# Kernel tuning notes

Hardware: AMD Instinct MI355X
Metric: run time of the kernel (lower is better)

## Reference

```python
import jax, jax.numpy as jnp
import numpy as np

L, B, Q, P, D, H, F = 3, 256, 128, 16, 256, 16, 512
DK = D // H
SCALE = DK ** -0.5  # lsa=False -> constant scale
EPS = 1e-5


def _ln(x, g, b):
    m = jnp.mean(x, axis=-1, keepdims=True)
    v = jnp.mean(jnp.square(x - m), axis=-1, keepdims=True)
    return (x - m) * jax.lax.rsqrt(v + EPS) * g + b


def setup_inputs() -> dict:
    key = jax.random.key(0)
    ks = jax.random.split(key, 12)
    w = lambda k, shape: 0.02 * jax.random.normal(k, shape, dtype=jnp.float32)
    return {
        "x": jax.random.normal(ks[0], (B, Q, P), dtype=jnp.float32),
        "attn_bias": 0.1 * jax.random.normal(ks[1], (1, Q, Q), dtype=jnp.float32),
        "W_P": w(ks[2], (P, D)), "b_P": jnp.zeros((D,), jnp.float32),
        "W_pos": w(ks[3], (Q, D)),
        "Wq": w(ks[4], (L, D, D)), "bq": jnp.zeros((L, D), jnp.float32),
        "Wk": w(ks[5], (L, D, D)), "bk": jnp.zeros((L, D), jnp.float32),
        "Wv": w(ks[6], (L, D, D)), "bv": jnp.zeros((L, D), jnp.float32),
        "Wo": w(ks[7], (L, D, D)), "bo": jnp.zeros((L, D), jnp.float32),
        "ln1_g": jnp.ones((L, D), jnp.float32), "ln1_b": jnp.zeros((L, D), jnp.float32),
        "W1": w(ks[8], (L, D, F)), "b1": jnp.zeros((L, F), jnp.float32),
        "W2": w(ks[9], (L, F, D)), "b2": jnp.zeros((L, D), jnp.float32),
        "ln2_g": jnp.ones((L, D), jnp.float32), "ln2_b": jnp.zeros((L, D), jnp.float32),
    }


def _encoder(x, attn_bias, W_P, b_P, W_pos,
             Wq, bq, Wk, bk, Wv, bv, Wo, bo, ln1_g, ln1_b,
             W1, b1, W2, b2, ln2_g, ln2_b):
    # patch embedding + positional encoding (dropout=0, eval mode)
    z = x @ W_P + b_P + W_pos                      # [B, Q, D]
    bias = attn_bias[:, None]                      # [1, 1, Q, Q]

    def layer(carry, p):
        z, prev = carry
        (wq, bq_, wk, bk_, wv, bv_, wo, bo_, g1, be1, w1, b1_, w2, b2_, g2, be2) = p
        q = (z @ wq + bq_).reshape(B, Q, H, DK).transpose(0, 2, 1, 3)  # [B,H,Q,dk]
        k = (z @ wk + bk_).reshape(B, Q, H, DK).transpose(0, 2, 1, 3)
        v = (z @ wv + bv_).reshape(B, Q, H, DK).transpose(0, 2, 1, 3)
        # residual-attention + bias-augmented scores
        scores = jnp.einsum('bhqd,bhkd->bhqk', q, k) * SCALE + prev + bias
        attn = jax.nn.softmax(scores, axis=-1)
        o = jnp.einsum('bhqk,bhkd->bhqd', attn, v)
        o = o.transpose(0, 2, 1, 3).reshape(B, Q, D) @ wo + bo_
        z = _ln(z + o, g1, be1)                     # post-norm
        ffo = jax.nn.gelu(z @ w1 + b1_, approximate=False) @ w2 + b2_
        z = _ln(z + ffo, g2, be2)
        return (z, scores), None

    prev0 = jnp.zeros((B, H, Q, Q), z.dtype)        # prev=None == add zero
    params = (Wq, bq, Wk, bk, Wv, bv, Wo, bo, ln1_g, ln1_b,
              W1, b1, W2, b2, ln2_g, ln2_b)
    (z, _), _ = jax.lax.scan(layer, (z, prev0), params)
    return z


def reference(x, attn_bias, W_P, b_P, W_pos, Wq, bq, Wk, bk, Wv, bv, Wo, bo,
              ln1_g, ln1_b, W1, b1, W2, b2, ln2_g, ln2_b):
    return _encoder(x, attn_bias, W_P, b_P, W_pos, Wq, bq, Wk, bk, Wv, bv,
                    Wo, bo, ln1_g, ln1_b, W1, b1, W2, b2, ln2_g, ln2_b)
```

## Files before the change

kernel.cpp:

```cpp
#include <hip/hip_runtime.h>

#define DEV __device__ __forceinline__

typedef float          f32x4  __attribute__((ext_vector_type(4)));
typedef __bf16         bf16x8 __attribute__((ext_vector_type(8)));
typedef unsigned short u16x8  __attribute__((ext_vector_type(8)));

static constexpr int  Bq   = 256;
static constexpr int  Qs   = 128;
static constexpr int  Dm   = 256;
static constexpr int  Ff   = 512;
static constexpr int  ROWS = Bq * Qs;
static constexpr long QK_LSTR = (long)ROWS * 512;

DEV float b2f(unsigned short h) {
    unsigned int u = ((unsigned int)h) << 16;
    float f; __builtin_memcpy(&f, &u, 4); return f;
}
DEV unsigned short f2b(float f) {
    unsigned int u; __builtin_memcpy(&u, &f, 4);
    u += 0x7fffu + ((u >> 16) & 1u);
    return (unsigned short)(u >> 16);
}
DEV f32x4 mfma_bf16(u16x8 a, u16x8 b, f32x4 c) {
    return __builtin_amdgcn_mfma_f32_16x16x32_bf16(
        __builtin_bit_cast(bf16x8, a), __builtin_bit_cast(bf16x8, b), c, 0, 0, 0);
}
DEV void gl_lds16(const unsigned short* g, unsigned short* l) {
    __builtin_amdgcn_global_load_lds(
        (const __attribute__((address_space(1))) unsigned int*)g,
        (__attribute__((address_space(3))) unsigned int*)l, 16, 0, 0);
}
DEV int zadr(int row, int col) {
    return row * 256 + ((((col >> 3) ^ (row & 7))) << 3) + (col & 7);
}

__global__ void k_embed(const float* __restrict__ x,
                        const float* __restrict__ WP,
                        const float* __restrict__ bP,
                        const float* __restrict__ Wpos,
                        unsigned short* __restrict__ zb) {
    int row = blockIdx.x;
    int d   = threadIdx.x;
    int q   = row & (Qs - 1);
    const float* xr = x + row * 16;
    float acc = bP[d] + Wpos[q * Dm + d];
#pragma unroll
    for (int p = 0; p < 16; p++) acc += xr[p] * WP[p * Dm + d];
    zb[(long)row * Dm + d] = f2b(acc);
}

static constexpr int S0 = 3 * 768 * 256;
static constexpr int S1 = 3 * 256 * 256;
static constexpr int S2 = 3 * 512 * 256;
static constexpr int S3 = 3 * 256 * 512;
static constexpr int S4 = 3 * 768;
static constexpr int S5 = 3 * 64 * 256;
static constexpr int PREP_TOT = S0 + S1 + S2 + S3 + S4 + S5;

__global__ void k_prep(const float* __restrict__ Wq, const float* __restrict__ Wk,
                       const float* __restrict__ Wv, const float* __restrict__ Wo,
                       const float* __restrict__ W1, const float* __restrict__ W2,
                       const float* __restrict__ bq, const float* __restrict__ bk,
                       const float* __restrict__ bv, const float* __restrict__ ab,
                       unsigned short* __restrict__ wTqkv, unsigned short* __restrict__ wTo,
                       unsigned short* __restrict__ wp1, unsigned short* __restrict__ wp2,
                       float* __restrict__ bqkv, float* __restrict__ pb) {
    int idx = blockIdx.x * 256 + threadIdx.x;
    if (idx < S0) {
        int l = idx / (768 * 256), r = idx % (768 * 256);
        int n = r / 256, k = r % 256;
        const float* W = (n < 256) ? Wq : (n < 512) ? Wk : Wv;
        float v = W[(long)l * 65536 + k * 256 + (n & 255)];
        if (n < 256) v *= 0.25f;
        wTqkv[idx] = f2b(v);
    } else if (idx < S0 + S1) {
        int j = idx - S0;
        int l = j / 65536, r = j % 65536, n = r / 256, k = r % 256;
        wTo[j] = f2b(Wo[(long)l * 65536 + k * 256 + n]);
    } else if (idx < S0 + S1 + S2) {
        int j = idx - S0 - S1;
        int l = j / 131072, r = j % 131072;
        int tile = r >> 9, le = r & 511, lane = le >> 3, e = le & 7;
        int ntile = tile >> 3, kk = tile & 7;
        int n = ntile * 16 + (lane & 15), k = kk * 32 + (lane >> 4) * 8 + e;
        wp1[j] = f2b(W1[(long)l * 131072 + k * 512 + n]);
    } else if (idx < S0 + S1 + S2 + S3) {
        int j = idx - S0 - S1 - S2;
        int l = j / 131072, r = j % 131072;
        int tile = r >> 9, le = r & 511, lane = le >> 3, e = le & 7;
        int ntile = tile >> 4, kk = tile & 15;
        int n = ntile * 16 + (lane & 15), k = kk * 32 + (lane >> 4) * 8 + e;
        wp2[j] = f2b(W2[(long)l * 131072 + k * 256 + n]);
    } else if (idx < S0 + S1 + S2 + S3 + S4) {
        int j = idx - S0 - S1 - S2 - S3;
        int l = j / 768, c = j % 768;
        float v = (c < 256) ? bq[l * 256 + c] * 0.25f
                : (c < 512) ? bk[l * 256 + c - 256]
                            : bv[l * 256 + c - 512];
        bqkv[j] = v;
    } else if (idx < PREP_TOT) {
        int j = idx - S0 - S1 - S2 - S3 - S4;
        int l = j / 16384, r = j % 16384;
        int u = r / 256, t = r % 256;
        int i = u >> 5, rr = (u >> 3) & 3, jj = u & 7;
        int wave = t >> 6, quad = (t >> 4) & 3, l16 = t & 15;
        int m = 32 * wave + 16 * i + 4 * quad + rr;
        int col = 16 * jj + l16;
        pb[j] = (float)(l + 1) * ab[m * 128 + col];
    }
}

template <int GELU, int MODE>
__global__ __launch_bounds__(256) void k_gemm(const unsigned short* __restrict__ A,
                                              const unsigned short* __restrict__ WT,
                                              const float* __restrict__ bias,
                                              unsigned short* __restrict__ outB,
                                              unsigned short* __restrict__ aux,
                                              int M, int N, int K) {
    __shared__ unsigned short smem[16384];
    unsigned short* As = smem;
    unsigned short* Bs = smem + 8192;
    const int tid  = threadIdx.x;
    const int wave = tid >> 6, lane = tid & 63, quad = lane >> 4, l16 = lane & 15;
    const int mq = wave >> 1, nq = wave & 1;
    const int m_blk = blockIdx.x * 128, n_blk = blockIdx.y * 128;
    const int c0 = tid, c1 = tid + 256;
    const int ra0 = c0 >> 2, ca0 = (c0 & 3) * 8;
    const int ra1 = c1 >> 2, ca1 = (c1 & 3) * 8;

    f32x4 acc[4][4] = {};

    for (int k0 = 0; k0 < K; k0 += 64) {
#pragma unroll
        for (int hh = 0; hh < 2; hh++) {
            int kk = k0 + hh * 32;
            gl_lds16(A  + (long)(m_blk + ra0) * K + kk + ca0, &As[hh * 4096 + c0 * 8]);
            gl_lds16(A  + (long)(m_blk + ra1) * K + kk + ca1, &As[hh * 4096 + c1 * 8]);
            gl_lds16(WT + (long)(n_blk + ra0) * K + kk + ca0, &Bs[hh * 4096 + c0 * 8]);
            gl_lds16(WT + (long)(n_blk + ra1) * K + kk + ca1, &Bs[hh * 4096 + c1 * 8]);
        }
        __syncthreads();
#pragma unroll
        for (int hh = 0; hh < 2; hh++) {
            u16x8 af[4], bf[4];
#pragma unroll
            for (int i = 0; i < 4; i++)
                af[i] = *(const u16x8*)&As[hh * 4096 + (64 * mq + 16 * i + l16) * 32 + quad * 8];
#pragma unroll
            for (int j = 0; j < 4; j++)
                bf[j] = *(const u16x8*)&Bs[hh * 4096 + (64 * nq + 16 * j + l16) * 32 + quad * 8];
#pragma unroll
            for (int i = 0; i < 4; i++)
#pragma unroll
                for (int j = 0; j < 4; j++)
                    acc[i][j] = mfma_bf16(af[i], bf[j], acc[i][j]);
        }
        __syncthreads();
    }

#pragma unroll
    for (int i = 0; i < 4; i++) {
        int rl = 64 * mq + 16 * i + quad * 4;
#pragma unroll
        for (int j = 0; j < 4; j++) {
            int cl = 64 * nq + 16 * j + l16;
            float bb = bias[n_blk + cl];
#pragma unroll
            for (int r = 0; r < 4; r++) {
                float v = acc[i][j][r] + bb;
                if (GELU) v = 0.5f * v * (1.0f + erff(v * 0.70710678118f));
                if (MODE == 0) smem[(rl + r) * 128 + cl] = f2b(v);
                if (MODE == 2) {
                    int g = 4 * nq + j;
                    smem[g * 2048 + (rl + r) * 16 + l16] = f2b(v);
                }
            }
        }
    }
    __syncthreads();
#pragma unroll
    for (int c = tid; c < 2048; c += 256) {
        u16x8 val = *(const u16x8*)&smem[c * 8];
        if (MODE == 0) {
            int row = c >> 4, seg = c & 15;
            *(u16x8*)&outB[(long)(m_blk + row) * N + n_blk + seg * 8] = val;
        }
        if (MODE == 2) {
            int g = c >> 8, w = c & 255;
            int n = n_blk + g * 16;
            if (n < 512) {
                int s = n >> 8, h = (n >> 4) & 15;
                *(u16x8*)&outB[((long)(((m_blk >> 7) * 16 + h) * 2 + s)) * 2048 + w * 8] = val;
            } else {
                int hh = (n - 512) >> 4;
                *(u16x8*)&aux[((long)hh * ROWS + m_blk) * 16 + w * 8] = val;
            }
        }
    }
}

template <int LAST, int AHM>
__global__ __launch_bounds__(256) void k_gemm_ln(const unsigned short* __restrict__ A,
                                                 const unsigned short* __restrict__ WT,
                                                 const float* __restrict__ bias,
                                                 const unsigned short* __restrict__ Zres,
                                                 const float* __restrict__ g,
                                                 const float* __restrict__ be,
                                                 unsigned short* __restrict__ zb,
                                                 float* __restrict__ outF,
                                                 int K) {
    __shared__ unsigned short smem[16384 + 2048 + 8192];
    unsigned short* Zs = smem;
    unsigned short* As = smem + 16384;
    unsigned short* Bs = smem + 16384 + 2048;
    float2* stats = (float2*)(smem + 16384);

    const int tid  = threadIdx.x;
    const int wave = tid >> 6, lane = tid & 63, quad = lane >> 4, l16 = lane & 15;
    const int m_blk = blockIdx.x * 64;

#pragma unroll
    for (int s = 0; s < 8; s++) {
        int c = tid + 256 * s;
        int zr = c >> 5, zc = (c & 31) * 8;
        gl_lds16(Zres + (long)(m_blk + zr) * 256 + zc, &Zs[c * 8]);
    }

    const int ca = (tid & 3) * 8, raA = tid >> 2;
    f32x4 acc[4][4] = {};

    for (int k0 = 0; k0 < K; k0 += 32) {
        if (AHM) {
            int k = k0 + ca;
            gl_lds16(A + ((long)(k >> 4) * ROWS + m_blk + raA) * 16 + (k & 15), &As[tid * 8]);
        } else {
            gl_lds16(A + (long)(m_blk + raA) * K + k0 + ca, &As[tid * 8]);
        }
#pragma unroll
        for (int s = 0; s < 4; s++) {
            int c = tid + 256 * s;
            int br = c >> 2, bc = (c & 3) * 8;
            gl_lds16(WT + (long)br * K + k0 + bc, &Bs[c * 8]);
        }
        __syncthreads();
        u16x8 af[4], bf[4];
#pragma unroll
        for (int i = 0; i < 4; i++)
            af[i] = *(const u16x8*)&As[(16 * i + l16) * 32 + quad * 8];
#pragma unroll
        for (int j = 0; j < 4; j++)
            bf[j] = *(const u16x8*)&Bs[(64 * wave + 16 * j + l16) * 32 + quad * 8];
#pragma unroll
        for (int i = 0; i < 4; i++)
#pragma unroll
            for (int j = 0; j < 4; j++)
                acc[i][j] = mfma_bf16(af[i], bf[j], acc[i][j]);
        __syncthreads();
    }

    float bb[4], gg[4], bt[4];
#pragma unroll
    for (int j = 0; j < 4; j++) {
        int col = 64 * wave + 16 * j + l16;
        bb[j] = bias[col]; gg[j] = g[col]; bt[j] = be[col];
    }
#pragma unroll
    for (int i = 0; i < 4; i++) {
#pragma unroll
        for (int r = 0; r < 4; r++) {
            int rloc = 16 * i + quad * 4 + r;
            float s1 = 0.f, s2 = 0.f;
#pragma unroll
            for (int j = 0; j < 4; j++) {
                int col = 64 * wave + 16 * j + l16;
                float v = acc[i][j][r] + bb[j] + b2f(Zs[rloc * 256 + col]);
                acc[i][j][r] = v;
                s1 += v; s2 += v * v;
            }
            for (int mk = 1; mk < 16; mk <<= 1) {
                s1 += __shfl_xor(s1, mk);
                s2 += __shfl_xor(s2, mk);
            }
            if (l16 == 0) stats[rloc * 4 + wave] = make_float2(s1, s2);
        }
    }
    __syncthreads();
#pragma unroll
    for (int i = 0; i < 4; i++) {
#pragma unroll
        for (int r = 0; r < 4; r++) {
            int rloc = 16 * i + quad * 4 + r;
            f32x4 p0 = *(const f32x4*)&stats[rloc * 4];
            f32x4 p1 = *(const f32x4*)&stats[rloc * 4 + 2];
            float S1 = p0[0] + p0[2] + p1[0] + p1[2];
            float S2 = p0[1] + p0[3] + p1[1] + p1[3];
            float mean = S1 * (1.0f / 256.0f);
            float var  = S2 * (1.0f / 256.0f) - mean * mean;
            float rstd = rsqrtf(var + 1e-5f);
            long grow = m_blk + rloc;
#pragma unroll
            for (int j = 0; j < 4; j++) {
                int col = 64 * wave + 16 * j + l16;
                float o = (acc[i][j][r] - mean) * rstd * gg[j] + bt[j];
                if (LAST) outF[grow * 256 + col] = o;
                else      zb[grow * 256 + col] = f2b(o);
            }
        }
    }
}

template <int LAST>
__global__ __launch_bounds__(256, 2) void k_ffn(const unsigned short* __restrict__ zin,
                                                const unsigned short* __restrict__ wp1,
                                                const float* __restrict__ b1,
                                                const unsigned short* __restrict__ wp2,
                                                const float* __restrict__ b2,
                                                const float* __restrict__ g2,
                                                const float* __restrict__ be2,
                                                unsigned short* __restrict__ zout,
                                                float* __restrict__ outF) {
    __shared__ unsigned short Zs[64 * 256];
    __shared__ unsigned short Hs[64 * 256];
    __shared__ float2 stats[64 * 4];

    const int tid  = threadIdx.x;
    const int wave = tid >> 6, lane = tid & 63, quad = (lane >> 4) & 3, l16 = lane & 15;
    const int m_blk = blockIdx.x * 64;

    {
        int row = tid >> 2;
#pragma unroll
        for (int cc = 0; cc < 8; cc++) {
            int c0 = (tid & 3) * 64 + cc * 8;
            u16x8 v = *(const u16x8*)&zin[(long)(m_blk + row) * 256 + c0];
            *(u16x8*)&Zs[zadr(row, c0)] = v;
        }
    }
    __syncthreads();

    f32x4 z2[4][4] = {};
#pragma unroll 1
    for (int c = 0; c < 2; c++) {
        f32x4 a1[4][4] = {};
#pragma unroll 2
        for (int kk = 0; kk < 8; kk++) {
            u16x8 af[4], bf[4];
#pragma unroll
            for (int i = 0; i < 4; i++)
                af[i] = *(const u16x8*)&Zs[(16 * i + l16) * 256 + (((kk * 4 + quad) ^ (l16 & 7)) << 3)];
#pragma unroll
            for (int j = 0; j < 4; j++)
                bf[j] = *(const u16x8*)&wp1[((long)(16 * c + 4 * wave + j) * 8 + kk) * 512 + lane * 8];
#pragma unroll
            for (int i = 0; i < 4; i++)
#pragma unroll
                for (int j = 0; j < 4; j++)
                    a1[i][j] = mfma_bf16(af[i], bf[j], a1[i][j]);
        }
        __syncthreads();
        float b1v[4];
#pragma unroll
        for (int j = 0; j < 4; j++) b1v[j] = b1[256 * c + 64 * wave + 16 * j + l16];
#pragma unroll
        for (int i = 0; i < 4; i++)
#pragma unroll
            for (int j = 0; j < 4; j++)
#pragma unroll
                for (int r = 0; r < 4; r++) {
                    int row  = 16 * i + quad * 4 + r;
                    int colh = 64 * wave + 16 * j + l16;
                    float v = a1[i][j][r] + b1v[j];
                    float gel = 0.5f * v * (1.0f + erff(v * 0.70710678118f));
                    Hs[zadr(row, colh)] = f2b(gel);
                }
        __syncthreads();
#pragma unroll 2
        for (int kk = 0; kk < 8; kk++) {
            u16x8 af[4], bf[4];
#pragma unroll
            for (int i = 0; i < 4; i++)
                af[i] = *(const u16x8*)&Hs[(16 * i + l16) * 256 + (((kk * 4 + quad) ^ (l16 & 7)) << 3)];
#pragma unroll
            for (int j = 0; j < 4; j++)
                bf[j] = *(const u16x8*)&wp2[((long)(4 * wave + j) * 16 + 8 * c + kk) * 512 + lane * 8];
#pragma unroll
            for (int i = 0; i < 4; i++)
#pragma unroll
                for (int j = 0; j < 4; j++)
                    z2[i][j] = mfma_bf16(af[i], bf[j], z2[i][j]);
        }
    }

    float b2v[4], gg[4], bb[4];
#pragma unroll
    for (int j = 0; j < 4; j++) {
        int col = 64 * wave + 16 * j + l16;
        b2v[j] = b2[col]; gg[j] = g2[col]; bb[j] = be2[col];
    }
#pragma unroll
    for (int i = 0; i < 4; i++)
#pragma unroll
        for (int r = 0; r < 4; r++) {
            int row = 16 * i + quad * 4 + r;
            float s1 = 0.f, s2 = 0.f;
#pragma unroll
            for (int j = 0; j < 4; j++) {
                int col = 64 * wave + 16 * j + l16;
                float v = z2[i][j][r] + b2v[j] + b2f(Zs[zadr(row, col)]);
                z2[i][j][r] = v; s1 += v; s2 += v * v;
            }
            for (int mk = 1; mk < 16; mk <<= 1) { s1 += __shfl_xor(s1, mk); s2 += __shfl_xor(s2, mk); }
            if (l16 == 0) stats[row * 4 + wave] = make_float2(s1, s2);
        }
    __syncthreads();
#pragma unroll
    for (int i = 0; i < 4; i++)
#pragma unroll
        for (int r = 0; r < 4; r++) {
            int row = 16 * i + quad * 4 + r;
            f32x4 p0 = *(const f32x4*)&stats[row * 4];
            f32x4 p1 = *(const f32x4*)&stats[row * 4 + 2];
            float S1 = p0[0] + p0[2] + p1[0] + p1[2];
            float S2 = p0[1] + p0[3] + p1[1] + p1[3];
            float mean = S1 * (1.0f / 256.0f);
            float var  = S2 * (1.0f / 256.0f) - mean * mean;
            float rstd = rsqrtf(var + 1e-5f);
            long grow = m_blk + row;
#pragma unroll
            for (int j = 0; j < 4; j++) {
                int col = 64 * wave + 16 * j + l16;
                float o = (z2[i][j][r] - mean) * rstd * gg[j] + bb[j];
                if (LAST) outF[grow * 256 + col] = o;
                else      zout[grow * 256 + col] = f2b(o);
            }
        }
}

template <int L>
__global__ __launch_bounds__(256) void k_attn(const unsigned short* __restrict__ qkh,
                                              const unsigned short* __restrict__ vbuf,
                                              const float* __restrict__ pb,
                                              unsigned short* __restrict__ o_out) {
    __shared__ unsigned short vt[16 * 136];
    __shared__ unsigned short Ps[128 * 136];
    const int tid  = threadIdx.x;
    const int wave = tid >> 6, lane = tid & 63, quad = lane >> 4, l16 = lane & 15;
    const int b = blockIdx.x >> 4, h = blockIdx.x & 15;
    const int qrow = tid >> 1, half = tid & 1;

    u16x8 vv = *(const u16x8*)(vbuf + ((long)h * ROWS + b * Qs + qrow) * 16 + half * 8);
    const float* pbt = pb + (long)L * 16384 + tid;

    f32x4 accS[2][8] = {};
    u16x8 zero = {};

    constexpr int FULL = (L + 1) / 2;
    constexpr bool HALF = ((L + 1) & 1) != 0;

#pragma unroll
    for (int p = 0; p < FULL; p++) {
        const unsigned short* q0 = qkh + ((long)(((2 * p) * Bq + b) * 16 + h) * 2) * 2048;
        const unsigned short* q1 = qkh + ((long)(((2 * p + 1) * Bq + b) * 16 + h) * 2) * 2048;
        const unsigned short* qsel = (quad < 2) ? q0 : q1;
        const unsigned short* ksel = (quad < 2) ? (q0 + 2048) : (q1 + 2048);
        const int koff = (quad & 1) * 8;
        u16x8 af[2], bf8[8];
#pragma unroll
        for (int i = 0; i < 2; i++) {
            int m = 32 * wave + 16 * i + l16;
            af[i] = *(const u16x8*)(qsel + m * 16 + koff);
        }
#pragma unroll
        for (int j = 0; j < 8; j++) {
            int n = 16 * j + l16;
            bf8[j] = *(const u16x8*)(ksel + n * 16 + koff);
        }
#pragma unroll
        for (int i = 0; i < 2; i++)
#pragma unroll
            for (int j = 0; j < 8; j++)
                accS[i][j] = mfma_bf16(af[i], bf8[j], accS[i][j]);
    }
    if (HALF) {
        const unsigned short* qt = qkh + ((long)((L * Bq + b) * 16 + h) * 2) * 2048;
        const unsigned short* kt = qt + 2048;
        u16x8 af[2], bf8[8];
#pragma unroll
        for (int i = 0; i < 2; i++) {
            int m = 32 * wave + 16 * i + l16;
            af[i] = (quad < 2) ? *(const u16x8*)(qt + m * 16 + quad * 8) : zero;
        }
#pragma unroll
        for (int j = 0; j < 8; j++) {
            int n = 16 * j + l16;
            bf8[j] = (quad < 2) ? *(const u16x8*)(kt + n * 16 + quad * 8) : zero;
        }
#pragma unroll
        for (int i = 0; i < 2; i++)
#pragma unroll
            for (int j = 0; j < 8; j++)
                accS[i][j] = mfma_bf16(af[i], bf8[j], accS[i][j]);
    }

#pragma unroll
    for (int jj = 0; jj < 8; jj++) vt[(half * 8 + jj) * 136 + qrow] = vv[jj];

#pragma unroll
    for (int i = 0; i < 2; i++) {
#pragma unroll
        for (int r = 0; r < 4; r++) {
            int m = 32 * wave + 16 * i + quad * 4 + r;
#pragma unroll
            for (int j = 0; j < 8; j++) {
                int u = (i * 4 + r) * 8 + j;
                float s = accS[i][j][r] + pbt[u * 256];
                Ps[m * 136 + 16 * j + l16] = f2b(__expf(s));
            }
        }
    }
    __syncthreads();

    f32x4 accO[2] = {};
    f32x4 accR[2] = {};
    u16x8 ones;
#pragma unroll
    for (int jj = 0; jj < 8; jj++) ones[jj] = 0x3F80;
#pragma unroll
    for (int s = 0; s < 4; s++) {
        u16x8 bv = *(const u16x8*)&vt[l16 * 136 + s * 32 + quad * 8];
#pragma unroll
        for (int i = 0; i < 2; i++) {
            u16x8 ap = *(const u16x8*)&Ps[(32 * wave + 16 * i + l16) * 136 + s * 32 + quad * 8];
            accO[i] = mfma_bf16(ap, bv, accO[i]);
            accR[i] = mfma_bf16(ap, ones, accR[i]);
        }
    }
    __syncthreads();
#pragma unroll
    for (int i = 0; i < 2; i++)
#pragma unroll
        for (int r = 0; r < 4; r++) {
            int m = 32 * wave + 16 * i + quad * 4 + r;
            float inv = __builtin_amdgcn_rcpf(accR[i][r]);
            vt[m * 16 + l16] = f2b(accO[i][r] * inv);
        }
    __syncthreads();
    {
        unsigned short* obase = o_out + ((long)h * ROWS + b * Qs) * 16;
        *(u16x8*)&obase[tid * 8] = *(const u16x8*)&vt[tid * 8];
    }
}

extern "C" void kernel_launch(void* const* d_in, const int* in_sizes, int n_in,
                              void* d_out, int out_size, void* d_ws, size_t ws_size,
                              hipStream_t stream) {
    const float* x     = (const float*)d_in[0];
    const float* abias = (const float*)d_in[1];
    const float* WP    = (const float*)d_in[2];
    const float* bP    = (const float*)d_in[3];
    const float* Wpos  = (const float*)d_in[4];
    const float* Wq    = (const float*)d_in[5];
    const float* bqp   = (const float*)d_in[6];
    const float* Wk    = (const float*)d_in[7];
    const float* bkp   = (const float*)d_in[8];
    const float* Wv    = (const float*)d_in[9];
    const float* bvp   = (const float*)d_in[10];
    const float* Wo    = (const float*)d_in[11];
    const float* bo    = (const float*)d_in[12];
    const float* g1    = (const float*)d_in[13];
    const float* be1   = (const float*)d_in[14];
    const float* W1    = (const float*)d_in[15];
    const float* b1    = (const float*)d_in[16];
    const float* W2    = (const float*)d_in[17];
    const float* b2    = (const float*)d_in[18];
    const float* g2    = (const float*)d_in[19];
    const float* be2   = (const float*)d_in[20];
    (void)in_sizes; (void)n_in; (void)out_size; (void)ws_size;

    char* ws = (char*)d_ws;
    size_t off = 0;
    auto alloc = [&](size_t bytes) -> char* {
        char* p = ws + off; off += (bytes + 255) & ~(size_t)255; return p;
    };
    unsigned short* z_b   = (unsigned short*)alloc((size_t)ROWS * Dm * 2);
    unsigned short* qkh   = (unsigned short*)alloc((size_t)3 * ROWS * 512 * 2);
    unsigned short* v_cur = (unsigned short*)alloc((size_t)ROWS * Dm * 2);
    unsigned short* o_b   = (unsigned short*)alloc((size_t)ROWS * Dm * 2);
    unsigned short* wTqkv = (unsigned short*)alloc((size_t)S0 * 2);
    unsigned short* wTo   = (unsigned short*)alloc((size_t)S1 * 2);
    unsigned short* wp1   = (unsigned short*)alloc((size_t)S2 * 2);
    unsigned short* wp2   = (unsigned short*)alloc((size_t)S3 * 2);
    float*          bqkv  = (float*)alloc((size_t)S4 * 4);
    float*          pb    = (float*)alloc((size_t)S5 * 4);

    k_prep<<<(PREP_TOT + 255) / 256, 256, 0, stream>>>(
        Wq, Wk, Wv, Wo, W1, W2, bqp, bkp, bvp, abias,
        wTqkv, wTo, wp1, wp2, bqkv, pb);
    k_embed<<<ROWS, 256, 0, stream>>>(x, WP, bP, Wpos, z_b);

    for (int l = 0; l < 3; l++) {
        k_gemm<0, 2><<<dim3(ROWS / 128, 6), 256, 0, stream>>>(
            z_b, wTqkv + (long)l * 768 * 256, bqkv + l * 768,
            qkh + (long)l * QK_LSTR, v_cur, ROWS, 768, 256);
        if (l == 0)      k_attn<0><<<Bq * 16, 256, 0, stream>>>(qkh, v_cur, pb, o_b);
        else if (l == 1) k_attn<1><<<Bq * 16, 256, 0, stream>>>(qkh, v_cur, pb, o_b);
        else             k_attn<2><<<Bq * 16, 256, 0, stream>>>(qkh, v_cur, pb, o_b);
        k_gemm_ln<0, 1><<<ROWS / 64, 256, 0, stream>>>(
            o_b, wTo + (long)l * 256 * 256, bo + l * 256, z_b,
            g1 + l * 256, be1 + l * 256, z_b, nullptr, 256);
        if (l == 2)
            k_ffn<1><<<ROWS / 64, 256, 0, stream>>>(
                z_b, wp1 + (long)l * 131072, b1 + l * 512,
                wp2 + (long)l * 131072, b2 + l * 256,
                g2 + l * 256, be2 + l * 256, nullptr, (float*)d_out);
        else
            k_ffn<0><<<ROWS / 64, 256, 0, stream>>>(
                z_b, wp1 + (long)l * 131072, b1 + l * 512,
                wp2 + (long)l * 131072, b2 + l * 256,
                g2 + l * 256, be2 + l * 256, z_b, nullptr);
    }
}
```

Baseline: 500.3 us.

## Fuse QKV projection into FFN kernel epilogue and embedding into first pass

Removes the standalone QKV GEMM and embedding kernels. The QKV projection for the next layer now runs inside the FFN kernel on the freshly normalized rows still held in shared memory, and a MODE 0 variant computes the patch embedding before doing the layer-0 QKV projection. The FFN kernel moves to 512 threads with 8 waves, prepacked MFMA-layout weights and double-buffered weight fragments. This saves a round trip of z through global memory and several launches, in exchange for higher register pressure, direct uncoalesced 16-bit stores of q/k/v from registers, and weights now read straight from global rather than staged in LDS.

```diff
diff --git a/kernel.cpp b/kernel.cpp
--- a/kernel.cpp
+++ b/kernel.cpp
@@ -33,21 +33,6 @@
 }
 DEV int zadr(int row, int col) {
     return row * 256 + ((((col >> 3) ^ (row & 7))) << 3) + (col & 7);
-}
-
-__global__ void k_embed(const float* __restrict__ x,
-                        const float* __restrict__ WP,
-                        const float* __restrict__ bP,
-                        const float* __restrict__ Wpos,
-                        unsigned short* __restrict__ zb) {
-    int row = blockIdx.x;
-    int d   = threadIdx.x;
-    int q   = row & (Qs - 1);
-    const float* xr = x + row * 16;
-    float acc = bP[d] + Wpos[q * Dm + d];
-#pragma unroll
-    for (int p = 0; p < 16; p++) acc += xr[p] * WP[p * Dm + d];
-    zb[(long)row * Dm + d] = f2b(acc);
 }
 
 static constexpr int S0 = 3 * 768 * 256;
@@ -63,17 +48,20 @@
                        const float* __restrict__ W1, const float* __restrict__ W2,
                        const float* __restrict__ bq, const float* __restrict__ bk,
                        const float* __restrict__ bv, const float* __restrict__ ab,
-                       unsigned short* __restrict__ wTqkv, unsigned short* __restrict__ wTo,
+                       unsigned short* __restrict__ wpQ, unsigned short* __restrict__ wTo,
                        unsigned short* __restrict__ wp1, unsigned short* __restrict__ wp2,
                        float* __restrict__ bqkv, float* __restrict__ pb) {
     int idx = blockIdx.x * 256 + threadIdx.x;
     if (idx < S0) {
-        int l = idx / (768 * 256), r = idx % (768 * 256);
-        int n = r / 256, k = r % 256;
-        const float* W = (n < 256) ? Wq : (n < 512) ? Wk : Wv;
-        float v = W[(long)l * 65536 + k * 256 + (n & 255)];
-        if (n < 256) v *= 0.25f;
-        wTqkv[idx] = f2b(v);
+        int l = idx / 196608, r = idx % 196608;
+        int tile = r >> 9, le = r & 511, lane = le >> 3, e = le & 7;
+        int ntile = tile >> 3, kk = tile & 7;
+        int n = ntile * 16 + (lane & 15), k = kk * 32 + (lane >> 4) * 8 + e;
+        float v;
+        if (n < 256)      v = Wq[(long)l * 65536 + k * 256 + n] * 0.25f;
+        else if (n < 512) v = Wk[(long)l * 65536 + k * 256 + (n - 256)];
+        else              v = Wv[(long)l * 65536 + k * 256 + (n - 512)];
+        wpQ[idx] = f2b(v);
     } else if (idx < S0 + S1) {
         int j = idx - S0;
         int l = j / 65536, r = j % 65536, n = r / 256, k = r % 256;
@@ -111,95 +99,6 @@
     }
 }
 
-template <int GELU, int MODE>
-__global__ __launch_bounds__(256) void k_gemm(const unsigned short* __restrict__ A,
-                                              const unsigned short* __restrict__ WT,
-                                              const float* __restrict__ bias,
-                                              unsigned short* __restrict__ outB,
-                                              unsigned short* __restrict__ aux,
-                                              int M, int N, int K) {
-    __shared__ unsigned short smem[16384];
-    unsigned short* As = smem;
-    unsigned short* Bs = smem + 8192;
-    const int tid  = threadIdx.x;
-    const int wave = tid >> 6, lane = tid & 63, quad = lane >> 4, l16 = lane & 15;
-    const int mq = wave >> 1, nq = wave & 1;
-    const int m_blk = blockIdx.x * 128, n_blk = blockIdx.y * 128;
-    const int c0 = tid, c1 = tid + 256;
-    const int ra0 = c0 >> 2, ca0 = (c0 & 3) * 8;
-    const int ra1 = c1 >> 2, ca1 = (c1 & 3) * 8;
-
-    f32x4 acc[4][4] = {};
-
-    for (int k0 = 0; k0 < K; k0 += 64) {
-#pragma unroll
-        for (int hh = 0; hh < 2; hh++) {
-            int kk = k0 + hh * 32;
-            gl_lds16(A  + (long)(m_blk + ra0) * K + kk + ca0, &As[hh * 4096 + c0 * 8]);
-            gl_lds16(A  + (long)(m_blk + ra1) * K + kk + ca1, &As[hh * 4096 + c1 * 8]);
-            gl_lds16(WT + (long)(n_blk + ra0) * K + kk + ca0, &Bs[hh * 4096 + c0 * 8]);
-            gl_lds16(WT + (long)(n_blk + ra1) * K + kk + ca1, &Bs[hh * 4096 + c1 * 8]);
-        }
-        __syncthreads();
-#pragma unroll
-        for (int hh = 0; hh < 2; hh++) {
-            u16x8 af[4], bf[4];
-#pragma unroll
-            for (int i = 0; i < 4; i++)
-                af[i] = *(const u16x8*)&As[hh * 4096 + (64 * mq + 16 * i + l16) * 32 + quad * 8];
-#pragma unroll
-            for (int j = 0; j < 4; j++)
-                bf[j] = *(const u16x8*)&Bs[hh * 4096 + (64 * nq + 16 * j + l16) * 32 + quad * 8];
-#pragma unroll
-            for (int i = 0; i < 4; i++)
-#pragma unroll
-                for (int j = 0; j < 4; j++)
-                    acc[i][j] = mfma_bf16(af[i], bf[j], acc[i][j]);
-        }
-        __syncthreads();
-    }
-
-#pragma unroll
-    for (int i = 0; i < 4; i++) {
-        int rl = 64 * mq + 16 * i + quad * 4;
-#pragma unroll
-        for (int j = 0; j < 4; j++) {
-            int cl = 64 * nq + 16 * j + l16;
-            float bb = bias[n_blk + cl];
-#pragma unroll
-            for (int r = 0; r < 4; r++) {
-                float v = acc[i][j][r] + bb;
-                if (GELU) v = 0.5f * v * (1.0f + erff(v * 0.70710678118f));
-                if (MODE == 0) smem[(rl + r) * 128 + cl] = f2b(v);
-                if (MODE == 2) {
-                    int g = 4 * nq + j;
-                    smem[g * 2048 + (rl + r) * 16 + l16] = f2b(v);
-                }
-            }
-        }
-    }
-    __syncthreads();
-#pragma unroll
-    for (int c = tid; c < 2048; c += 256) {
-        u16x8 val = *(const u16x8*)&smem[c * 8];
-        if (MODE == 0) {
-            int row = c >> 4, seg = c & 15;
-            *(u16x8*)&outB[(long)(m_blk + row) * N + n_blk + seg * 8] = val;
-        }
-        if (MODE == 2) {
-            int g = c >> 8, w = c & 255;
-            int n = n_blk + g * 16;
-            if (n < 512) {
-                int s = n >> 8, h = (n >> 4) & 15;
-                *(u16x8*)&outB[((long)(((m_blk >> 7) * 16 + h) * 2 + s)) * 2048 + w * 8] = val;
-            } else {
-                int hh = (n - 512) >> 4;
-                *(u16x8*)&aux[((long)hh * ROWS + m_blk) * 16 + w * 8] = val;
-            }
-        }
-    }
-}
-
 template <int LAST, int AHM>
 __global__ __launch_bounds__(256) void k_gemm_ln(const unsigned short* __restrict__ A,
                                                  const unsigned short* __restrict__ WT,
@@ -310,131 +209,229 @@
     }
 }
 
-template <int LAST>
-__global__ __launch_bounds__(256, 2) void k_ffn(const unsigned short* __restrict__ zin,
-                                                const unsigned short* __restrict__ wp1,
-                                                const float* __restrict__ b1,
-                                                const unsigned short* __restrict__ wp2,
-                                                const float* __restrict__ b2,
-                                                const float* __restrict__ g2,
-                                                const float* __restrict__ be2,
-                                                unsigned short* __restrict__ zout,
-                                                float* __restrict__ outF) {
+template <int MODE>
+__global__ __launch_bounds__(512, 4) void k_ffn(
+    const float* __restrict__ x, const float* __restrict__ WP,
+    const float* __restrict__ bP, const float* __restrict__ Wpos,
+    const unsigned short* __restrict__ zin, unsigned short* __restrict__ zout,
+    const unsigned short* __restrict__ wp1, const float* __restrict__ b1,
+    const unsigned short* __restrict__ wp2, const float* __restrict__ b2,
+    const float* __restrict__ g2, const float* __restrict__ be2,
+    const unsigned short* __restrict__ wpQ, const float* __restrict__ bq,
+    unsigned short* __restrict__ qkh, unsigned short* __restrict__ vcur,
+    float* __restrict__ outF) {
     __shared__ unsigned short Zs[64 * 256];
     __shared__ unsigned short Hs[64 * 256];
-    __shared__ float2 stats[64 * 4];
+    float2* stats = (float2*)Hs;
 
     const int tid  = threadIdx.x;
-    const int wave = tid >> 6, lane = tid & 63, quad = (lane >> 4) & 3, l16 = lane & 15;
+    const int lane = tid & 63, quad = (lane >> 4) & 3, l16 = lane & 15;
+    const int wave = tid >> 6, wr = wave >> 2, wc = wave & 3;
     const int m_blk = blockIdx.x * 64;
 
-    {
-        int row = tid >> 2;
-#pragma unroll
-        for (int cc = 0; cc < 8; cc++) {
-            int c0 = (tid & 3) * 64 + cc * 8;
-            u16x8 v = *(const u16x8*)&zin[(long)(m_blk + row) * 256 + c0];
-            *(u16x8*)&Zs[zadr(row, c0)] = v;
-        }
-    }
-    __syncthreads();
-
-    f32x4 z2[4][4] = {};
+    if constexpr (MODE == 0) {
+        int row = tid >> 3;
+        long grow = m_blk + row;
+        int q = (int)(grow & (Qs - 1));
+        const float* xr = x + grow * 16;
+        float xl[16];
+#pragma unroll
+        for (int p = 0; p < 16; p++) xl[p] = xr[p];
+        int cbase = (tid & 7) * 32;
+#pragma unroll
+        for (int cc = 0; cc < 4; cc++) {
+            int c0 = cbase + cc * 8;
+            u16x8 pk;
+#pragma unroll
+            for (int e = 0; e < 8; e++) {
+                int c = c0 + e;
+                float a = bP[c] + Wpos[q * 256 + c];
+#pragma unroll
+                for (int p = 0; p < 16; p++) a += xl[p] * WP[p * 256 + c];
+                pk[e] = f2b(a);
+            }
+            *(u16x8*)&Zs[zadr(row, c0)] = pk;
+            *(u16x8*)&zout[grow * 256 + c0] = pk;
+        }
+        __syncthreads();
+    } else {
+#pragma unroll
+        for (int s = 0; s < 4; s++) {
+            int c = tid + 512 * s;
+            int zr = c >> 5, zc = (c & 31) * 8;
+            u16x8 v = *(const u16x8*)&zin[(long)(m_blk + zr) * 256 + zc];
+            *(u16x8*)&Zs[zadr(zr, zc)] = v;
+        }
+        __syncthreads();
+    }
+
+    if constexpr (MODE >= 1) {
+        f32x4 z2[2][4] = {};
 #pragma unroll 1
-    for (int c = 0; c < 2; c++) {
-        f32x4 a1[4][4] = {};
-#pragma unroll 2
-        for (int kk = 0; kk < 8; kk++) {
-            u16x8 af[4], bf[4];
-#pragma unroll
-            for (int i = 0; i < 4; i++)
-                af[i] = *(const u16x8*)&Zs[(16 * i + l16) * 256 + (((kk * 4 + quad) ^ (l16 & 7)) << 3)];
+        for (int c = 0; c < 2; c++) {
+            f32x4 a1[2][4] = {};
+            u16x8 bf[2][4];
 #pragma unroll
             for (int j = 0; j < 4; j++)
-                bf[j] = *(const u16x8*)&wp1[((long)(16 * c + 4 * wave + j) * 8 + kk) * 512 + lane * 8];
-#pragma unroll
-            for (int i = 0; i < 4; i++)
+                bf[0][j] = *(const u16x8*)&wp1[((long)(16 * c + 4 * wc + j) * 8 + 0) * 512 + lane * 8];
+#pragma unroll
+            for (int kk = 0; kk < 8; kk++) {
+                if (kk < 7)
+#pragma unroll
+                    for (int j = 0; j < 4; j++)
+                        bf[(kk + 1) & 1][j] = *(const u16x8*)&wp1[((long)(16 * c + 4 * wc + j) * 8 + kk + 1) * 512 + lane * 8];
+                u16x8 af[2];
+#pragma unroll
+                for (int i = 0; i < 2; i++)
+                    af[i] = *(const u16x8*)&Zs[(32 * wr + 16 * i + l16) * 256 + (((kk * 4 + quad) ^ (l16 & 7)) << 3)];
+#pragma unroll
+                for (int i = 0; i < 2; i++)
+#pragma unroll
+                    for (int j = 0; j < 4; j++)
+                        a1[i][j] = mfma_bf16(af[i], bf[kk & 1][j], a1[i][j]);
+            }
+            __syncthreads();
+            float b1v[4];
+#pragma unroll
+            for (int j = 0; j < 4; j++) b1v[j] = b1[256 * c + 64 * wc + 16 * j + l16];
+#pragma unroll
+            for (int i = 0; i < 2; i++)
 #pragma unroll
                 for (int j = 0; j < 4; j++)
-                    a1[i][j] = mfma_bf16(af[i], bf[j], a1[i][j]);
+#pragma unroll
+                    for (int r = 0; r < 4; r++) {
+                        int row  = 32 * wr + 16 * i + quad * 4 + r;
+                        int colh = 64 * wc + 16 * j + l16;
+                        float v = a1[i][j][r] + b1v[j];
+                        float gel = 0.5f * v * (1.0f + erff(v * 0.70710678118f));
+                        Hs[zadr(row, colh)] = f2b(gel);
+                    }
+            __syncthreads();
+            u16x8 bg[2][4];
+#pragma unroll
+            for (int j = 0; j < 4; j++)
+                bg[0][j] = *(const u16x8*)&wp2[((long)(4 * wc + j) * 16 + 8 * c + 0) * 512 + lane * 8];
+#pragma unroll
+            for (int kk = 0; kk < 8; kk++) {
+                if (kk < 7)
+#pragma unroll
+                    for (int j = 0; j < 4; j++)
+                        bg[(kk + 1) & 1][j] = *(const u16x8*)&wp2[((long)(4 * wc + j) * 16 + 8 * c + kk + 1) * 512 + lane * 8];
+                u16x8 af[2];
+#pragma unroll
+                for (int i = 0; i < 2; i++)
+                    af[i] = *(const u16x8*)&Hs[(32 * wr + 16 * i + l16) * 256 + (((kk * 4 + quad) ^ (l16 & 7)) << 3)];
+#pragma unroll
+                for (int i = 0; i < 2; i++)
+#pragma unroll
+                    for (int j = 0; j < 4; j++)
+                        z2[i][j] = mfma_bf16(af[i], bg[kk & 1][j], z2[i][j]);
+            }
         }
         __syncthreads();
-        float b1v[4];
-#pragma unroll
-        for (int j = 0; j < 4; j++) b1v[j] = b1[256 * c + 64 * wave + 16 * j + l16];
-#pragma unroll
-        for (int i = 0; i < 4; i++)
-#pragma unroll
-            for (int j = 0; j < 4; j++)
-#pragma unroll
-                for (int r = 0; r < 4; r++) {
-                    int row  = 16 * i + quad * 4 + r;
-                    int colh = 64 * wave + 16 * j + l16;
-                    float v = a1[i][j][r] + b1v[j];
-                    float gel = 0.5f * v * (1.0f + erff(v * 0.70710678118f));
-                    Hs[zadr(row, colh)] = f2b(gel);
+
+        float b2v[4], gg[4], bb[4];
+#pragma unroll
+        for (int j = 0; j < 4; j++) {
+            int col = 64 * wc + 16 * j + l16;
+            b2v[j] = b2[col]; gg[j] = g2[col]; bb[j] = be2[col];
+        }
+#pragma unroll
+        for (int i = 0; i < 2; i++)
+#pragma unroll
+            for (int r = 0; r < 4; r++) {
+                int row = 32 * wr + 16 * i + quad * 4 + r;
+                float s1 = 0.f, s2 = 0.f;
+#pragma unroll
+                for (int j = 0; j < 4; j++) {
+                    int col = 64 * wc + 16 * j + l16;
+                    float v = z2[i][j][r] + b2v[j] + b2f(Zs[zadr(row, col)]);
+                    z2[i][j][r] = v; s1 += v; s2 += v * v;
                 }
+                for (int mk = 1; mk < 16; mk <<= 1) { s1 += __shfl_xor(s1, mk); s2 += __shfl_xor(s2, mk); }
+                if (l16 == 0) stats[row * 4 + wc] = make_float2(s1, s2);
+            }
         __syncthreads();
-#pragma unroll 2
-        for (int kk = 0; kk < 8; kk++) {
-            u16x8 af[4], bf[4];
-#pragma unroll
-            for (int i = 0; i < 4; i++)
-                af[i] = *(const u16x8*)&Hs[(16 * i + l16) * 256 + (((kk * 4 + quad) ^ (l16 & 7)) << 3)];
-#pragma unroll
-            for (int j = 0; j < 4; j++)
-                bf[j] = *(const u16x8*)&wp2[((long)(4 * wave + j) * 16 + 8 * c + kk) * 512 + lane * 8];
-#pragma unroll
-            for (int i = 0; i < 4; i++)
-#pragma unroll
-                for (int j = 0; j < 4; j++)
-                    z2[i][j] = mfma_bf16(af[i], bf[j], z2[i][j]);
-        }
-    }
-
-    float b2v[4], gg[4], bb[4];
-#pragma unroll
-    for (int j = 0; j < 4; j++) {
-        int col = 64 * wave + 16 * j + l16;
-        b2v[j] = b2[col]; gg[j] = g2[col]; bb[j] = be2[col];
-    }
-#pragma unroll
-    for (int i = 0; i < 4; i++)
-#pragma unroll
-        for (int r = 0; r < 4; r++) {
-            int row = 16 * i + quad * 4 + r;
-            float s1 = 0.f, s2 = 0.f;
-#pragma unroll
-            for (int j = 0; j < 4; j++) {
-                int col = 64 * wave + 16 * j + l16;
-                float v = z2[i][j][r] + b2v[j] + b2f(Zs[zadr(row, col)]);
-                z2[i][j][r] = v; s1 += v; s2 += v * v;
-            }
-            for (int mk = 1; mk < 16; mk <<= 1) { s1 += __shfl_xor(s1, mk); s2 += __shfl_xor(s2, mk); }
-            if (l16 == 0) stats[row * 4 + wave] = make_float2(s1, s2);
-        }
-    __syncthreads();
-#pragma unroll
-    for (int i = 0; i < 4; i++)
-#pragma unroll
-        for (int r = 0; r < 4; r++) {
-            int row = 16 * i + quad * 4 + r;
-            f32x4 p0 = *(const f32x4*)&stats[row * 4];
-            f32x4 p1 = *(const f32x4*)&stats[row * 4 + 2];
-            float S1 = p0[0] + p0[2] + p1[0] + p1[2];
-            float S2 = p0[1] + p0[3] + p1[1] + p1[3];
-            float mean = S1 * (1.0f / 256.0f);
-            float var  = S2 * (1.0f / 256.0f) - mean * mean;
-            float rstd = rsqrtf(var + 1e-5f);
-            long grow = m_blk + row;
-#pragma unroll
-            for (int j = 0; j < 4; j++) {
-                int col = 64 * wave + 16 * j + l16;
-                float o = (z2[i][j][r] - mean) * rstd * gg[j] + bb[j];
-                if (LAST) outF[grow * 256 + col] = o;
-                else      zout[grow * 256 + col] = f2b(o);
-            }
-        }
+#pragma unroll
+        for (int i = 0; i < 2; i++)
+#pragma unroll
+            for (int r = 0; r < 4; r++) {
+                int row = 32 * wr + 16 * i + quad * 4 + r;
+                f32x4 p0 = *(const f32x4*)&stats[row * 4];
+                f32x4 p1 = *(const f32x4*)&stats[row * 4 + 2];
+                float S1 = p0[0] + p0[2] + p1[0] + p1[2];
+                float S2 = p0[1] + p0[3] + p1[1] + p1[3];
+                float mean = S1 * (1.0f / 256.0f);
+                float var  = S2 * (1.0f / 256.0f) - mean * mean;
+                float rstd = rsqrtf(var + 1e-5f);
+                long grow = m_blk + row;
+#pragma unroll
+                for (int j = 0; j < 4; j++) {
+                    int col = 64 * wc + 16 * j + l16;
+                    float o = (z2[i][j][r] - mean) * rstd * gg[j] + bb[j];
+                    if constexpr (MODE == 2) {
+                        outF[grow * 256 + col] = o;
+                    } else {
+                        unsigned short hv = f2b(o);
+                        Zs[zadr(row, col)] = hv;
+                        zout[grow * 256 + col] = hv;
+                    }
+                }
+            }
+        if constexpr (MODE == 1) __syncthreads();
+    }
+
+    if constexpr (MODE <= 1) {
+#pragma unroll 1
+        for (int p = 0; p < 2; p++) {
+            f32x4 aq[2][6] = {};
+            u16x8 bf[2][6];
+#pragma unroll
+            for (int j = 0; j < 6; j++)
+                bf[0][j] = *(const u16x8*)&wpQ[((long)(24 * p + 6 * wc + j) * 8 + 0) * 512 + lane * 8];
+#pragma unroll
+            for (int kk = 0; kk < 8; kk++) {
+                if (kk < 7)
+#pragma unroll
+                    for (int j = 0; j < 6; j++)
+                        bf[(kk + 1) & 1][j] = *(const u16x8*)&wpQ[((long)(24 * p + 6 * wc + j) * 8 + kk + 1) * 512 + lane * 8];
+                u16x8 af[2];
+#pragma unroll
+                for (int i = 0; i < 2; i++)
+                    af[i] = *(const u16x8*)&Zs[(32 * wr + 16 * i + l16) * 256 + (((kk * 4 + quad) ^ (l16 & 7)) << 3)];
+#pragma unroll
+                for (int i = 0; i < 2; i++)
+#pragma unroll
+                    for (int j = 0; j < 6; j++)
+                        aq[i][j] = mfma_bf16(af[i], bf[kk & 1][j], aq[i][j]);
+            }
+#pragma unroll
+            for (int j = 0; j < 6; j++) {
+                int col = 384 * p + 96 * wc + 16 * j + l16;
+                float bqv = bq[col];
+                if (col < 512) {
+                    int s = col >> 8, hh = (col >> 4) & 15;
+                    unsigned short* qk = qkh + ((long)(((m_blk >> 7) * 16 + hh) * 2 + s)) * 2048;
+#pragma unroll
+                    for (int i = 0; i < 2; i++)
+#pragma unroll
+                        for (int r = 0; r < 4; r++) {
+                            int rin = (m_blk & 127) + 32 * wr + 16 * i + quad * 4 + r;
+                            qk[rin * 16 + l16] = f2b(aq[i][j][r] + bqv);
+                        }
+                } else {
+                    int hh = (col - 512) >> 4;
+#pragma unroll
+                    for (int i = 0; i < 2; i++)
+#pragma unroll
+                        for (int r = 0; r < 4; r++) {
+                            long grow = m_blk + 32 * wr + 16 * i + quad * 4 + r;
+                            vcur[((long)hh * ROWS + grow) * 16 + l16] = f2b(aq[i][j][r] + bqv);
+                        }
+                }
+            }
+        }
+    }
 }
 
 template <int L>
@@ -587,7 +584,7 @@
     unsigned short* qkh   = (unsigned short*)alloc((size_t)3 * ROWS * 512 * 2);
     unsigned short* v_cur = (unsigned short*)alloc((size_t)ROWS * Dm * 2);
     unsigned short* o_b   = (unsigned short*)alloc((size_t)ROWS * Dm * 2);
-    unsigned short* wTqkv = (unsigned short*)alloc((size_t)S0 * 2);
+    unsigned short* wpQ   = (unsigned short*)alloc((size_t)S0 * 2);
     unsigned short* wTo   = (unsigned short*)alloc((size_t)S1 * 2);
     unsigned short* wp1   = (unsigned short*)alloc((size_t)S2 * 2);
     unsigned short* wp2   = (unsigned short*)alloc((size_t)S3 * 2);
@@ -596,28 +593,34 @@
 
     k_prep<<<(PREP_TOT + 255) / 256, 256, 0, stream>>>(
         Wq, Wk, Wv, Wo, W1, W2, bqp, bkp, bvp, abias,
-        wTqkv, wTo, wp1, wp2, bqkv, pb);
-    k_embed<<<ROWS, 256, 0, stream>>>(x, WP, bP, Wpos, z_b);
+        wpQ, wTo, wp1, wp2, bqkv, pb);
+
+    k_ffn<0><<<ROWS / 64, 512, 0, stream>>>(
+        x, WP, bP, Wpos, nullptr, z_b,
+        nullptr, nullptr, nullptr, nullptr, nullptr, nullptr,
+        wpQ, bqkv, qkh, v_cur, nullptr);
 
     for (int l = 0; l < 3; l++) {
-        k_gemm<0, 2><<<dim3(ROWS / 128, 6), 256, 0, stream>>>(
-            z_b, wTqkv + (long)l * 768 * 256, bqkv + l * 768,
-            qkh + (long)l * QK_LSTR, v_cur, ROWS, 768, 256);
         if (l == 0)      k_attn<0><<<Bq * 16, 256, 0, stream>>>(qkh, v_cur, pb, o_b);
         else if (l == 1) k_attn<1><<<Bq * 16, 256, 0, stream>>>(qkh, v_cur, pb, o_b);
         else             k_attn<2><<<Bq * 16, 256, 0, stream>>>(qkh, v_cur, pb, o_b);
         k_gemm_ln<0, 1><<<ROWS / 64, 256, 0, stream>>>(
             o_b, wTo + (long)l * 256 * 256, bo + l * 256, z_b,
             g1 + l * 256, be1 + l * 256, z_b, nullptr, 256);
-        if (l == 2)
-            k_ffn<1><<<ROWS / 64, 256, 0, stream>>>(
-                z_b, wp1 + (long)l * 131072, b1 + l * 512,
+        if (l < 2)
+            k_ffn<1><<<ROWS / 64, 512, 0, stream>>>(
+                nullptr, nullptr, nullptr, nullptr, z_b, z_b,
+                wp1 + (long)l * 131072, b1 + l * 512,
                 wp2 + (long)l * 131072, b2 + l * 256,
-                g2 + l * 256, be2 + l * 256, nullptr, (float*)d_out);
+                g2 + l * 256, be2 + l * 256,
+                wpQ + (long)(l + 1) * 196608, bqkv + (l + 1) * 768,
+                qkh + (long)(l + 1) * QK_LSTR, v_cur, nullptr);
         else
-            k_ffn<0><<<ROWS / 64, 256, 0, stream>>>(
-                z_b, wp1 + (long)l * 131072, b1 + l * 512,
+            k_ffn<2><<<ROWS / 64, 512, 0, stream>>>(
+                nullptr, nullptr, nullptr, nullptr, z_b, nullptr,
+                wp1 + (long)l * 131072, b1 + l * 512,
                 wp2 + (long)l * 131072, b2 + l * 256,
-                g2 + l * 256, be2 + l * 256, z_b, nullptr);
-    }
-}
+                g2 + l * 256, be2 + l * 256,
+                nullptr, nullptr, nullptr, nullptr, (float*)d_out);
+    }
+}
```

Result: slower. 674.1 us (+34.7%).
